# Kernel tuning notes

Measured on AMD Instinct MI355X. Metric: run time of the kernel, lower is better.

The kernel has to match this reference:

```python
import jax, jax.numpy as jnp
import numpy as np

# corner sign pattern matching bbox_to_corners: x=[1,1,1,1,-1,-1,-1,-1], y=[1,1,-1,-1,1,1,-1,-1], z=[1,-1,1,-1,1,-1,1,-1]
CORNER_SIGNS = jnp.array(
    [[1., 1., 1.], [1., 1., -1.], [1., -1., 1.], [1., -1., -1.],
     [-1., 1., 1.], [-1., 1., -1.], [-1., -1., 1.], [-1., -1., -1.]],
    dtype=jnp.float32)


def _axis_rot(axis, a):
    """Rotation matrices (N,3,3) about a single axis, matching pytorch3d."""
    c, s = jnp.cos(a), jnp.sin(a)
    one, zero = jnp.ones_like(a), jnp.zeros_like(a)
    if axis == 'X':
        flat = (one, zero, zero, zero, c, -s, zero, s, c)
    elif axis == 'Y':
        flat = (c, zero, s, zero, one, zero, -s, zero, c)
    else:  # 'Z'
        flat = (c, -s, zero, s, c, zero, zero, zero, one)
    return jnp.stack(flat, axis=-1).reshape(a.shape + (3, 3))


def euler_zxy_to_matrix(angles):
    # convention 'ZXY': R = Rz(a0) @ Rx(a1) @ Ry(a2)
    Rz = _axis_rot('Z', angles[:, 0])
    Rx = _axis_rot('X', angles[:, 1])
    Ry = _axis_rot('Y', angles[:, 2])
    return Rz @ Rx @ Ry


def bbox_to_corners(bbox):
    """bbox (N,9) -> corners (N,8,3)."""
    centers = bbox[:, :3]
    half_sizes = bbox[:, 3:6] * 0.5
    rot = euler_zxy_to_matrix(bbox[:, 6:9])  # (N,3,3)
    corners = CORNER_SIGNS[None, :, :] * half_sizes[:, None, :]  # (N,8,3)
    # matmul(corners, rot^T): rotated[n,k,d] = sum_c corners[n,k,c] * rot[n,d,c]
    rotated = jnp.einsum('nkc,ndc->nkd', corners, rot)
    return centers[:, None, :] + rotated


def setup_inputs() -> dict:
    key = jax.random.key(0)
    k1, k2 = jax.random.split(key)
    N = 262144
    source = jax.random.normal(k1, (N, 9), dtype=jnp.float32)
    target = jax.random.normal(k2, (N, 9), dtype=jnp.float32)
    return {"source": source, "target": target}


def reference(source, target):
    # mode='l2' (mse per-element), group='g8', reduction='mean', loss_weight=1.0
    src_c = bbox_to_corners(source)  # (N,8,3)
    tgt_c = bbox_to_corners(target)  # (N,8,3)
    diff = src_c[:, :, None, :] - tgt_c[:, None, :, :]  # (N,8,8,3)
    dist = jnp.sum(diff * diff, axis=-1)  # (N,8,8): squared-L2 summed over coords
    # src->dst chamfer term only (dst_weight=0 and forward returns loss_source)
    loss_src = jnp.min(dist, axis=2)  # (N,8)
    loss = jnp.mean(loss_src) * 1.0  # forward loss_weight default * self.loss_weight
    return loss
```

## Files before the change

kernel.cpp:

```cpp
#include <hip/hip_runtime.h>

#define BLOCK 256

__device__ __forceinline__ void make_corners(const float* __restrict__ b, float c[24]) {
    const float px = b[0], py = b[1], pz = b[2];
    const float hx = 0.5f * b[3], hy = 0.5f * b[4], hz = 0.5f * b[5];
    const float az = b[6], ax = b[7], ay = b[8];
    float sz, cz, sx, cx, sy, cy;
    sincosf(az, &sz, &cz);
    sincosf(ax, &sx, &cx);
    sincosf(ay, &sy, &cy);
    const float u0 = hx * (cz * cy - sz * sx * sy);
    const float u1 = hx * (sz * cy + cz * sx * sy);
    const float u2 = hx * (-cx * sy);
    const float v0 = hy * (-sz * cx);
    const float v1 = hy * (cz * cx);
    const float v2 = hy * (sx);
    const float w0 = hz * (cz * sy + sz * sx * cy);
    const float w1 = hz * (sz * sy - cz * sx * cy);
    const float w2 = hz * (cx * cy);
#pragma unroll
    for (int k = 0; k < 8; ++k) {
        const float s0 = (k & 4) ? -1.f : 1.f;
        const float s1 = (k & 2) ? -1.f : 1.f;
        const float s2 = (k & 1) ? -1.f : 1.f;
        c[k * 3 + 0] = px + s0 * u0 + s1 * v0 + s2 * w0;
        c[k * 3 + 1] = py + s0 * u1 + s1 * v1 + s2 * w1;
        c[k * 3 + 2] = pz + s0 * u2 + s1 * v2 + s2 * w2;
    }
}

__global__ __launch_bounds__(BLOCK) void bbox_cd_partial(
    const float* __restrict__ src, const float* __restrict__ tgt,
    float* __restrict__ partial, int n) {
    __shared__ float s_src[BLOCK * 9];
    __shared__ float s_tgt[BLOCK * 9];

    const int block_base = blockIdx.x * BLOCK;
    const int nb = min(BLOCK, n - block_base);
    const int total = nb * 9;

    for (int i = threadIdx.x; i < total; i += BLOCK) {
        s_src[i] = src[block_base * 9 + i];
        s_tgt[i] = tgt[block_base * 9 + i];
    }
    __syncthreads();

    float lsum = 0.f;
    const int t = threadIdx.x;
    if (t < nb) {
        float sc[24], tc[24];
        make_corners(&s_src[t * 9], sc);
        make_corners(&s_tgt[t * 9], tc);
        float sum = 0.f;
#pragma unroll
        for (int i = 0; i < 8; ++i) {
            const float ax = sc[i * 3 + 0];
            const float ay = sc[i * 3 + 1];
            const float az = sc[i * 3 + 2];
            float best = 3.4e38f;
#pragma unroll
            for (int j = 0; j < 8; ++j) {
                const float dx = ax - tc[j * 3 + 0];
                const float dy = ay - tc[j * 3 + 1];
                const float dz = az - tc[j * 3 + 2];
                const float d = fmaf(dz, dz, fmaf(dy, dy, dx * dx));
                best = fminf(best, d);
            }
            sum += best;
        }
        lsum = sum;
    }

#pragma unroll
    for (int off = 32; off > 0; off >>= 1) lsum += __shfl_down(lsum, off, 64);

    __shared__ float wsum[BLOCK / 64];
    const int wave = threadIdx.x >> 6;
    const int lane = threadIdx.x & 63;
    if (lane == 0) wsum[wave] = lsum;
    __syncthreads();
    if (threadIdx.x == 0) {
        float b = 0.f;
#pragma unroll
        for (int w = 0; w < BLOCK / 64; ++w) b += wsum[w];
        partial[blockIdx.x] = b;
    }
}

__global__ __launch_bounds__(BLOCK) void bbox_cd_final(
    const float* __restrict__ partial, int nblocks, float* __restrict__ out,
    float inv_count) {
    float s = 0.f;
    for (int i = threadIdx.x; i < nblocks; i += BLOCK) s += partial[i];
#pragma unroll
    for (int off = 32; off > 0; off >>= 1) s += __shfl_down(s, off, 64);

    __shared__ float wsum[BLOCK / 64];
    const int wave = threadIdx.x >> 6;
    const int lane = threadIdx.x & 63;
    if (lane == 0) wsum[wave] = s;
    __syncthreads();
    if (threadIdx.x == 0) {
        float b = 0.f;
#pragma unroll
        for (int w = 0; w < BLOCK / 64; ++w) b += wsum[w];
        out[0] = b * inv_count;
    }
}

extern "C" void kernel_launch(void* const* d_in, const int* in_sizes, int n_in,
                              void* d_out, int out_size, void* d_ws, size_t ws_size,
                              hipStream_t stream) {
    const float* src = (const float*)d_in[0];
    const float* tgt = (const float*)d_in[1];
    float* out = (float*)d_out;
    const int n = in_sizes[0] / 9;
    const int nblocks = (n + BLOCK - 1) / BLOCK;

    float* partial = (float*)d_ws;

    bbox_cd_partial<<<nblocks, BLOCK, 0, stream>>>(src, tgt, partial, n);
    const float inv_count = 1.0f / (float)((long long)n * 8);
    bbox_cd_final<<<1, BLOCK, 0, stream>>>(partial, nblocks, out, inv_count);
}
```

Baseline: 14.14 us.

## Fuse final reduction via last-block atomic counter and use fast sincos

Merges the two-kernel reduction into one kernel: each block writes its partial sum, then bumps an atomic counter, and the last block to finish sums all partials and writes the mean. The goal is to remove the second kernel launch and its dependency gap. It adds a hipMemsetAsync per call to reset the counter, plus atomic traffic. It also switches sincosf to the lower-precision __sincosf intrinsic to cut transcendental cost.

```diff
diff --git a/kernel.cpp b/kernel.cpp
--- a/kernel.cpp
+++ b/kernel.cpp
@@ -7,9 +7,9 @@
     const float hx = 0.5f * b[3], hy = 0.5f * b[4], hz = 0.5f * b[5];
     const float az = b[6], ax = b[7], ay = b[8];
     float sz, cz, sx, cx, sy, cy;
-    sincosf(az, &sz, &cz);
-    sincosf(ax, &sx, &cx);
-    sincosf(ay, &sy, &cy);
+    __sincosf(az, &sz, &cz);
+    __sincosf(ax, &sx, &cx);
+    __sincosf(ay, &sy, &cy);
     const float u0 = hx * (cz * cy - sz * sx * sy);
     const float u1 = hx * (sz * cy + cz * sx * sy);
     const float u2 = hx * (-cx * sy);
@@ -30,9 +30,10 @@
     }
 }
 
-__global__ __launch_bounds__(BLOCK) void bbox_cd_partial(
+__global__ __launch_bounds__(BLOCK) void bbox_cd_fused(
     const float* __restrict__ src, const float* __restrict__ tgt,
-    float* __restrict__ partial, int n) {
+    unsigned int* __restrict__ counter, float* __restrict__ partials,
+    float* __restrict__ out, int n, float inv_count) {
     __shared__ float s_src[BLOCK * 9];
     __shared__ float s_tgt[BLOCK * 9];
 
@@ -76,6 +77,7 @@
     for (int off = 32; off > 0; off >>= 1) lsum += __shfl_down(lsum, off, 64);
 
     __shared__ float wsum[BLOCK / 64];
+    __shared__ int is_last;
     const int wave = threadIdx.x >> 6;
     const int lane = threadIdx.x & 63;
     if (lane == 0) wsum[wave] = lsum;
@@ -84,28 +86,29 @@
         float b = 0.f;
 #pragma unroll
         for (int w = 0; w < BLOCK / 64; ++w) b += wsum[w];
-        partial[blockIdx.x] = b;
+        __hip_atomic_store(&partials[blockIdx.x], b, __ATOMIC_RELAXED,
+                           __HIP_MEMORY_SCOPE_AGENT);
+        unsigned int old = __hip_atomic_fetch_add(counter, 1u, __ATOMIC_ACQ_REL,
+                                                  __HIP_MEMORY_SCOPE_AGENT);
+        is_last = (old == gridDim.x - 1) ? 1 : 0;
     }
-}
+    __syncthreads();
 
-__global__ __launch_bounds__(BLOCK) void bbox_cd_final(
-    const float* __restrict__ partial, int nblocks, float* __restrict__ out,
-    float inv_count) {
-    float s = 0.f;
-    for (int i = threadIdx.x; i < nblocks; i += BLOCK) s += partial[i];
+    if (is_last) {
+        float s = 0.f;
+        for (int i = threadIdx.x; i < (int)gridDim.x; i += BLOCK)
+            s += __hip_atomic_load(&partials[i], __ATOMIC_RELAXED,
+                                   __HIP_MEMORY_SCOPE_AGENT);
 #pragma unroll
-    for (int off = 32; off > 0; off >>= 1) s += __shfl_down(s, off, 64);
-
-    __shared__ float wsum[BLOCK / 64];
-    const int wave = threadIdx.x >> 6;
-    const int lane = threadIdx.x & 63;
-    if (lane == 0) wsum[wave] = s;
-    __syncthreads();
-    if (threadIdx.x == 0) {
-        float b = 0.f;
+        for (int off = 32; off > 0; off >>= 1) s += __shfl_down(s, off, 64);
+        if (lane == 0) wsum[wave] = s;
+        __syncthreads();
+        if (threadIdx.x == 0) {
+            float b = 0.f;
 #pragma unroll
-        for (int w = 0; w < BLOCK / 64; ++w) b += wsum[w];
-        out[0] = b * inv_count;
+            for (int w = 0; w < BLOCK / 64; ++w) b += wsum[w];
+            out[0] = b * inv_count;
+        }
     }
 }
 
@@ -118,9 +121,12 @@
     const int n = in_sizes[0] / 9;
     const int nblocks = (n + BLOCK - 1) / BLOCK;
 
-    float* partial = (float*)d_ws;
+    unsigned int* counter = (unsigned int*)d_ws;
+    float* partials = (float*)((char*)d_ws + 16);
 
-    bbox_cd_partial<<<nblocks, BLOCK, 0, stream>>>(src, tgt, partial, n);
+    hipMemsetAsync(d_ws, 0, 4, stream);
+
     const float inv_count = 1.0f / (float)((long long)n * 8);
-    bbox_cd_final<<<1, BLOCK, 0, stream>>>(partial, nblocks, out, inv_count);
+    bbox_cd_fused<<<nblocks, BLOCK, 0, stream>>>(src, tgt, counter, partials,
+                                                 out, n, inv_count);
 }
```

New measurement: 31.71 us. 2.24x slower.

## Exploit box corner symmetry to halve distance work, use fast sincos and vector loads

Applied to the files above, without the earlier changes.

Each box is now represented by its center and three half-axis vectors, not eight explicit corners. The squared distances are expanded algebraically so that corner pairs of the form ±c and ±r share terms, and each min is taken as R - |G±H|. This roughly halves the inner distance arithmetic. The change also switches to fast __sincosf intrinsics and loads full blocks into shared memory with float4. The cancellation-based expansion and the approximate sincos may change float rounding relative to the direct corner differences.

```diff
diff --git a/kernel.cpp b/kernel.cpp
--- a/kernel.cpp
+++ b/kernel.cpp
@@ -2,32 +2,25 @@
 
 #define BLOCK 256
 
-__device__ __forceinline__ void make_corners(const float* __restrict__ b, float c[24]) {
-    const float px = b[0], py = b[1], pz = b[2];
+__device__ __forceinline__ void make_frame(const float* __restrict__ b,
+                                           float p[3], float u[3], float v[3],
+                                           float w[3]) {
+    p[0] = b[0]; p[1] = b[1]; p[2] = b[2];
     const float hx = 0.5f * b[3], hy = 0.5f * b[4], hz = 0.5f * b[5];
     const float az = b[6], ax = b[7], ay = b[8];
     float sz, cz, sx, cx, sy, cy;
-    sincosf(az, &sz, &cz);
-    sincosf(ax, &sx, &cx);
-    sincosf(ay, &sy, &cy);
-    const float u0 = hx * (cz * cy - sz * sx * sy);
-    const float u1 = hx * (sz * cy + cz * sx * sy);
-    const float u2 = hx * (-cx * sy);
-    const float v0 = hy * (-sz * cx);
-    const float v1 = hy * (cz * cx);
-    const float v2 = hy * (sx);
-    const float w0 = hz * (cz * sy + sz * sx * cy);
-    const float w1 = hz * (sz * sy - cz * sx * cy);
-    const float w2 = hz * (cx * cy);
-#pragma unroll
-    for (int k = 0; k < 8; ++k) {
-        const float s0 = (k & 4) ? -1.f : 1.f;
-        const float s1 = (k & 2) ? -1.f : 1.f;
-        const float s2 = (k & 1) ? -1.f : 1.f;
-        c[k * 3 + 0] = px + s0 * u0 + s1 * v0 + s2 * w0;
-        c[k * 3 + 1] = py + s0 * u1 + s1 * v1 + s2 * w1;
-        c[k * 3 + 2] = pz + s0 * u2 + s1 * v2 + s2 * w2;
-    }
+    __sincosf(az, &sz, &cz);
+    __sincosf(ax, &sx, &cx);
+    __sincosf(ay, &sy, &cy);
+    u[0] = hx * (cz * cy - sz * sx * sy);
+    u[1] = hx * (sz * cy + cz * sx * sy);
+    u[2] = hx * (-cx * sy);
+    v[0] = hy * (-sz * cx);
+    v[1] = hy * (cz * cx);
+    v[2] = hy * (sx);
+    w[0] = hz * (cz * sy + sz * sx * cy);
+    w[1] = hz * (sz * sy - cz * sx * cy);
+    w[2] = hz * (cx * cy);
 }
 
 __global__ __launch_bounds__(BLOCK) void bbox_cd_partial(
@@ -38,36 +31,75 @@
 
     const int block_base = blockIdx.x * BLOCK;
     const int nb = min(BLOCK, n - block_base);
-    const int total = nb * 9;
 
-    for (int i = threadIdx.x; i < total; i += BLOCK) {
-        s_src[i] = src[block_base * 9 + i];
-        s_tgt[i] = tgt[block_base * 9 + i];
+    if (nb == BLOCK) {
+        const float4* s4 = reinterpret_cast<const float4*>(src + (size_t)block_base * 9);
+        const float4* t4 = reinterpret_cast<const float4*>(tgt + (size_t)block_base * 9);
+        float4* ds = reinterpret_cast<float4*>(s_src);
+        float4* dt = reinterpret_cast<float4*>(s_tgt);
+#pragma unroll
+        for (int i = threadIdx.x; i < (BLOCK * 9) / 4; i += BLOCK) {
+            ds[i] = s4[i];
+            dt[i] = t4[i];
+        }
+    } else {
+        for (int i = threadIdx.x; i < nb * 9; i += BLOCK) {
+            s_src[i] = src[(size_t)block_base * 9 + i];
+            s_tgt[i] = tgt[(size_t)block_base * 9 + i];
+        }
     }
     __syncthreads();
 
     float lsum = 0.f;
     const int t = threadIdx.x;
     if (t < nb) {
-        float sc[24], tc[24];
-        make_corners(&s_src[t * 9], sc);
-        make_corners(&s_tgt[t * 9], tc);
+        float ps[3], us[3], vs[3], ws_[3];
+        float pt[3], ut[3], vt[3], wt[3];
+        make_frame(&s_src[t * 9], ps, us, vs, ws_);
+        make_frame(&s_tgt[t * 9], pt, ut, vt, wt);
+
+        const float d0 = ps[0] - pt[0];
+        const float d1 = ps[1] - pt[1];
+        const float d2c = ps[2] - pt[2];
+        const float dd = fmaf(d0, d0, fmaf(d1, d1, d2c * d2c));
+        const float e0 = d0 + d0, e1 = d1 + d1, e2 = d2c + d2c;
+
+        float r[4][3], Rj[4], Gj[4];
+#pragma unroll
+        for (int j = 0; j < 4; ++j) {
+            const float s1 = (j & 2) ? -1.f : 1.f;
+            const float s2 = (j & 1) ? -1.f : 1.f;
+#pragma unroll
+            for (int k = 0; k < 3; ++k)
+                r[j][k] = ut[k] + s1 * vt[k] + s2 * wt[k];
+            Rj[j] = fmaf(r[j][0], r[j][0],
+                         fmaf(r[j][1], r[j][1], r[j][2] * r[j][2]));
+            Gj[j] = fmaf(e0, r[j][0], fmaf(e1, r[j][1], e2 * r[j][2]));
+        }
+
         float sum = 0.f;
 #pragma unroll
-        for (int i = 0; i < 8; ++i) {
-            const float ax = sc[i * 3 + 0];
-            const float ay = sc[i * 3 + 1];
-            const float az = sc[i * 3 + 2];
-            float best = 3.4e38f;
+        for (int i = 0; i < 4; ++i) {
+            const float s1 = (i & 2) ? -1.f : 1.f;
+            const float s2 = (i & 1) ? -1.f : 1.f;
+            float c0, c1, c2;
+            c0 = us[0] + s1 * vs[0] + s2 * ws_[0];
+            c1 = us[1] + s1 * vs[1] + s2 * ws_[1];
+            c2 = us[2] + s1 * vs[2] + s2 * ws_[2];
+            const float cc = fmaf(c0, c0, fmaf(c1, c1, c2 * c2));
+            const float A = dd + cc;
+            const float f0 = c0 + c0, f1 = c1 + c1, f2 = c2 + c2;
+            float bestP = 3.4e38f, bestM = 3.4e38f;
 #pragma unroll
-            for (int j = 0; j < 8; ++j) {
-                const float dx = ax - tc[j * 3 + 0];
-                const float dy = ay - tc[j * 3 + 1];
-                const float dz = az - tc[j * 3 + 2];
-                const float d = fmaf(dz, dz, fmaf(dy, dy, dx * dx));
-                best = fminf(best, d);
+            for (int j = 0; j < 4; ++j) {
+                const float H = fmaf(f0, r[j][0],
+                                     fmaf(f1, r[j][1], f2 * r[j][2]));
+                const float t1 = Gj[j] + H;
+                const float t2 = Gj[j] - H;
+                bestP = fminf(bestP, Rj[j] - fabsf(t1));
+                bestM = fminf(bestM, Rj[j] - fabsf(t2));
             }
-            sum += best;
+            sum += (A + A) + bestP + bestM;
         }
         lsum = sum;
     }
```

Measured after the change: 12.26 us. -13.3%, faster.
